# Performance work log

Measured on AMD Instinct MI355X. Metric: run time of the kernel, lower is better.

Reference implementation:

```python
import jax, jax.numpy as jnp
import numpy as np

B, S, D = 4, 4096, 1024
DD = 4 * D
N_EXPERTS = 8
CAPACITY = 1.0
LN_EPS = 1e-5


def setup_inputs() -> dict:
    key = jax.random.key(0)
    ks = jax.random.split(key, 8)
    s1 = 1.0 / np.sqrt(D)
    s2 = 1.0 / np.sqrt(DD)
    return {
        "x": jax.random.normal(ks[0], (B, S, D), jnp.float32),
        "gate_w": jax.random.normal(ks[1], (N_EXPERTS, D), jnp.float32) * 0.02,
        "ln_w": jnp.ones((D,), jnp.float32),
        "ln_b": jnp.zeros((D,), jnp.float32),
        "fc1s": jax.random.normal(ks[2], (N_EXPERTS, DD, D), jnp.float32) * s1,
        "b1s": jax.random.normal(ks[3], (N_EXPERTS, DD), jnp.float32) * s1,
        "fc2s": jax.random.normal(ks[4], (N_EXPERTS, D, DD), jnp.float32) * s2,
        "b2s": jax.random.normal(ks[5], (N_EXPERTS, D), jnp.float32) * s2,
    }


def reference(x, gate_w, ln_w, ln_b, fc1s, b1s, fc2s, b2s):
    og_shape = x.shape
    d = og_shape[-1]
    xf = x.reshape(-1, d)                       # (bs, d)
    bs = xf.shape[0]
    n = gate_w.shape[0]
    k = int(bs * CAPACITY) // n                 # static capacity per expert

    # softmax gating over experts
    scores = jax.nn.softmax(xf @ gate_w.T, axis=-1)   # (bs, n)

    # per-expert top-k tokens (column-wise descending sort, take first k)
    vals, idx = jax.lax.top_k(scores.T, k)      # (n, k)
    kept_w = vals.T                              # (k, n)
    kept_idx = idx.T                             # (k, n)
    flat_idx = kept_idx.reshape(-1)              # (k*n,) row-major: k outer, n inner

    # gather selected tokens, layernorm
    y = xf[flat_idx].reshape(k, n, d)            # (k, n, d)
    mu = y.mean(-1, keepdims=True)
    var = ((y - mu) ** 2).mean(-1, keepdims=True)
    y = (y - mu) * jax.lax.rsqrt(var + LN_EPS) * ln_w + ln_b

    # per-expert grouped GEMMs
    h = jnp.einsum('knd,nfd->knf', y, fc1s) + b1s          # (k, n, dd)
    h = jax.nn.gelu(h, approximate=True)                   # tanh gelu
    out = jnp.einsum('knf,ndf->knd', h, fc2s) + b2s        # (k, n, d)

    # weight by gate scores and scatter-add back onto the input tokens
    out = out * kept_w[..., None]
    xf = xf.at[flat_idx].add(out.reshape(k * n, d))
    return xf.reshape(og_shape)
```

## Files before the change

kernel.cpp:

```cpp
#include <hip/hip_runtime.h>

#define TOK  16384
#define NEXP 8
#define DIM  1024
#define DDIM 4096
#define KCAP 2048

typedef float  floatx4 __attribute__((ext_vector_type(4)));
typedef short  shortx8 __attribute__((ext_vector_type(8)));

static __device__ __forceinline__ unsigned short f2bf(float x) {
  unsigned u = __float_as_uint(x);
  return (unsigned short)((u + 0x7fffu + ((u >> 16) & 1u)) >> 16);
}

__global__ __launch_bounds__(256) void cvt_kernel(const float* __restrict__ src,
                                                  unsigned short* __restrict__ dst, int n4) {
  int i = blockIdx.x * 256 + threadIdx.x;
  if (i < n4) {
    float4 v = ((const float4*)src)[i];
    ushort4 o = make_ushort4(f2bf(v.x), f2bf(v.y), f2bf(v.z), f2bf(v.w));
    ((ushort4*)dst)[i] = o;
  }
}

__global__ __launch_bounds__(256) void gate_kernel(const float* __restrict__ x,
                                                   const float* __restrict__ gw,
                                                   float* __restrict__ scores) {
  __shared__ float gws[NEXP * DIM];
  int tid = threadIdx.x;
  for (int i = tid; i < NEXP * DIM / 4; i += 256)
    ((float4*)gws)[i] = ((const float4*)gw)[i];
  __syncthreads();
  int wave = tid >> 6, lane = tid & 63;
  int t = blockIdx.x * 4 + wave;
  const float4* xr = (const float4*)(x + (size_t)t * DIM);
  float4 xv[4];
#pragma unroll
  for (int j = 0; j < 4; ++j) xv[j] = xr[j * 64 + lane];
  float acc[NEXP];
#pragma unroll
  for (int e = 0; e < NEXP; ++e) acc[e] = 0.f;
#pragma unroll
  for (int e = 0; e < NEXP; ++e) {
    const float4* g4 = (const float4*)(gws + e * DIM);
#pragma unroll
    for (int j = 0; j < 4; ++j) {
      float4 g = g4[j * 64 + lane];
      acc[e] += xv[j].x * g.x + xv[j].y * g.y + xv[j].z * g.z + xv[j].w * g.w;
    }
  }
#pragma unroll
  for (int off = 32; off > 0; off >>= 1) {
#pragma unroll
    for (int e = 0; e < NEXP; ++e) acc[e] += __shfl_down(acc[e], off);
  }
  if (lane == 0) {
    float mx = acc[0];
#pragma unroll
    for (int e = 1; e < NEXP; ++e) mx = fmaxf(mx, acc[e]);
    float ex[NEXP], sum = 0.f;
#pragma unroll
    for (int e = 0; e < NEXP; ++e) { ex[e] = expf(acc[e] - mx); sum += ex[e]; }
    float inv = 1.f / sum;
#pragma unroll
    for (int e = 0; e < NEXP; ++e) scores[(size_t)e * TOK + t] = ex[e] * inv;
  }
}

#define TKT 1024
#define TKW (TKT / 64)
__global__ __launch_bounds__(TKT) void topk_kernel(const float* __restrict__ scores,
                                                   int* __restrict__ sel,
                                                   float* __restrict__ selw) {
  int e = blockIdx.x;
  const float* s = scores + (size_t)e * TOK;
  int tid = threadIdx.x, lane = tid & 63, wave = tid >> 6;
  __shared__ int cnt;
  __shared__ int wsum[TKW];

  unsigned prefix = 0;
  for (int bit = 30; bit >= 0; --bit) {
    unsigned cand = prefix | (1u << bit);
    if (tid == 0) cnt = 0;
    __syncthreads();
    int c = 0;
    for (int i = tid; i < TOK; i += TKT) c += (__float_as_uint(s[i]) >= cand) ? 1 : 0;
#pragma unroll
    for (int off = 32; off > 0; off >>= 1) c += __shfl_down(c, off);
    if (lane == 0) atomicAdd(&cnt, c);
    __syncthreads();
    if (cnt >= KCAP) prefix = cand;
    __syncthreads();
  }
  unsigned T = prefix;

  if (tid == 0) cnt = 0;
  __syncthreads();
  {
    int c = 0;
    for (int i = tid; i < TOK; i += TKT) c += (__float_as_uint(s[i]) > T) ? 1 : 0;
#pragma unroll
    for (int off = 32; off > 0; off >>= 1) c += __shfl_down(c, off);
    if (lane == 0) atomicAdd(&cnt, c);
  }
  __syncthreads();
  int n_gt = cnt;
  int need = KCAP - n_gt;

  __shared__ int pos;
  __shared__ int tiebase;
  if (tid == 0) { pos = 0; tiebase = 0; }
  __syncthreads();
  for (int chunk = 0; chunk < TOK; chunk += TKT) {
    int i = chunk + tid;
    unsigned v = __float_as_uint(s[i]);
    if (v > T) {
      int p = atomicAdd(&pos, 1);
      sel[e * KCAP + p]  = i;
      selw[e * KCAP + p] = __uint_as_float(v);
    }
    bool tie = (v == T);
    unsigned long long m = __ballot(tie);
    if (lane == 0) wsum[wave] = __popcll(m);
    __syncthreads();
    int base = tiebase;
    for (int w = 0; w < wave; ++w) base += wsum[w];
    int rank = base + __popcll(m & ((1ull << lane) - 1ull));
    if (tie && rank < need) {
      sel[e * KCAP + n_gt + rank]  = i;
      selw[e * KCAP + n_gt + rank] = __uint_as_float(T);
    }
    __syncthreads();
    if (tid == 0) {
      int tb = 0;
#pragma unroll
      for (int w = 0; w < TKW; ++w) tb += wsum[w];
      tiebase += tb;
    }
    __syncthreads();
  }
}

__global__ __launch_bounds__(256) void gather_ln_kernel(const float* __restrict__ x,
                                                        const int* __restrict__ sel,
                                                        const float* __restrict__ lnw,
                                                        const float* __restrict__ lnb,
                                                        unsigned short* __restrict__ Y) {
  int e = blockIdx.y, i = blockIdx.x;
  int tid = threadIdx.x, lane = tid & 63, wave = tid >> 6;
  int t = sel[e * KCAP + i];
  const float4* xr = (const float4*)(x + (size_t)t * DIM);
  float4 v = xr[tid];
  float s  = v.x + v.y + v.z + v.w;
  float sq = v.x * v.x + v.y * v.y + v.z * v.z + v.w * v.w;
#pragma unroll
  for (int off = 32; off > 0; off >>= 1) { s += __shfl_down(s, off); sq += __shfl_down(sq, off); }
  __shared__ float red[8];
  if (lane == 0) { red[wave] = s; red[4 + wave] = sq; }
  __syncthreads();
  s  = red[0] + red[1] + red[2] + red[3];
  sq = red[4] + red[5] + red[6] + red[7];
  float mu  = s * (1.f / DIM);
  float var = sq * (1.f / DIM) - mu * mu;
  float rs  = rsqrtf(var + 1e-5f);
  float4 w = ((const float4*)lnw)[tid];
  float4 b = ((const float4*)lnb)[tid];
  ushort4 o = make_ushort4(f2bf((v.x - mu) * rs * w.x + b.x),
                           f2bf((v.y - mu) * rs * w.y + b.y),
                           f2bf((v.z - mu) * rs * w.z + b.z),
                           f2bf((v.w - mu) * rs * w.w + b.w));
  ((ushort4*)(Y + ((size_t)e * KCAP + i) * DIM))[tid] = o;
}

#define BM  128
#define BN  128
#define BKT 64

template <int MODE>
__global__ __launch_bounds__(256) void gemm_kernel(
    const unsigned short* __restrict__ Aall,
    const unsigned short* __restrict__ Ball,
    const float* __restrict__ biasAll,
    int M, int N, int K,
    unsigned short* __restrict__ Hall,
    float* __restrict__ Out,
    const int* __restrict__ sel, const float* __restrict__ selw) {
  int e = blockIdx.z;
  const unsigned short* A = Aall + (size_t)e * M * K;
  const unsigned short* B = Ball + (size_t)e * N * K;
  const float* bias = biasAll + (size_t)e * N;

  __shared__ __align__(16) unsigned short As[BM * BKT];
  __shared__ __align__(16) unsigned short Bs[BN * BKT];
  __shared__ int   selS[BM];
  __shared__ float wS[BM];

  int tid = threadIdx.x, lane = tid & 63, wave = tid >> 6;
  int m0 = blockIdx.y * BM, n0 = blockIdx.x * BN;
  if (MODE == 2 && tid < BM) {
    selS[tid] = sel[e * KCAP + m0 + tid];
    wS[tid]   = selw[e * KCAP + m0 + tid];
  }
  int wm = (wave & 1) * 64, wn = (wave >> 1) * 64;
  int r8 = lane >> 3;
  int j8 = lane & 7;
  int scol = (j8 ^ r8) * 8;
  int row = lane & 15, quad = lane >> 4;
  int r7 = row & 7;

  floatx4 acc[4][4];
  floatx4 zero = {0.f, 0.f, 0.f, 0.f};
#pragma unroll
  for (int a = 0; a < 4; ++a)
#pragma unroll
    for (int b = 0; b < 4; ++b) acc[a][b] = zero;

  for (int k0 = 0; k0 < K; k0 += BKT) {
    __syncthreads();
#pragma unroll
    for (int j = 0; j < 4; ++j) {
      int q = wave * 4 + j;
      const unsigned short* ga = A + (size_t)(m0 + q * 8 + r8) * K + k0 + scol;
      __builtin_amdgcn_global_load_lds((const __attribute__((address_space(1))) void*)ga,
                                       (__attribute__((address_space(3))) void*)(As + q * 512),
                                       16, 0, 0);
      const unsigned short* gb = B + (size_t)(n0 + q * 8 + r8) * K + k0 + scol;
      __builtin_amdgcn_global_load_lds((const __attribute__((address_space(1))) void*)gb,
                                       (__attribute__((address_space(3))) void*)(Bs + q * 512),
                                       16, 0, 0);
    }
    __syncthreads();
#pragma unroll
    for (int kk = 0; kk < BKT; kk += 32) {
      int xg = ((quad + (kk >> 3)) ^ r7) << 3;
      shortx8 af[4], bf[4];
#pragma unroll
      for (int ti = 0; ti < 4; ++ti)
        af[ti] = *(const shortx8*)&As[(wm + ti * 16 + row) * BKT + xg];
#pragma unroll
      for (int tj = 0; tj < 4; ++tj)
        bf[tj] = *(const shortx8*)&Bs[(wn + tj * 16 + row) * BKT + xg];
#pragma unroll
      for (int ti = 0; ti < 4; ++ti)
#pragma unroll
        for (int tj = 0; tj < 4; ++tj)
          acc[ti][tj] = __builtin_amdgcn_mfma_f32_16x16x32_bf16(af[ti], bf[tj], acc[ti][tj], 0, 0, 0);
    }
  }

#pragma unroll
  for (int ti = 0; ti < 4; ++ti) {
#pragma unroll
    for (int tj = 0; tj < 4; ++tj) {
      int gn = n0 + wn + tj * 16 + row;
      float bb = bias[gn];
#pragma unroll
      for (int r = 0; r < 4; ++r) {
        int lrow = wm + ti * 16 + quad * 4 + r;
        float v = acc[ti][tj][r] + bb;
        if (MODE == 1) {
          float u = 0.7978845608028654f * (v + 0.044715f * v * v * v);
          u = fminf(u, 15.f);
          float e2 = __expf(2.f * u);
          float th = __fdividef(e2 - 1.f, e2 + 1.f);
          float g = 0.5f * v * (1.f + th);
          Hall[(size_t)e * M * N + (size_t)(m0 + lrow) * N + gn] = f2bf(g);
        } else {
          atomicAdd(&Out[(size_t)selS[lrow] * DIM + gn], wS[lrow] * v);
        }
      }
    }
  }
}

extern "C" void kernel_launch(void* const* d_in, const int* in_sizes, int n_in,
                              void* d_out, int out_size, void* d_ws, size_t ws_size,
                              hipStream_t stream) {
  const float* x   = (const float*)d_in[0];
  const float* gw  = (const float*)d_in[1];
  const float* lnw = (const float*)d_in[2];
  const float* lnb = (const float*)d_in[3];
  const float* fc1 = (const float*)d_in[4];
  const float* b1  = (const float*)d_in[5];
  const float* fc2 = (const float*)d_in[6];
  const float* b2  = (const float*)d_in[7];
  float* out = (float*)d_out;

  char* p = (char*)d_ws;
  float* scores = (float*)p;                 p += (size_t)NEXP * TOK * 4;
  int*   sel    = (int*)p;                   p += (size_t)NEXP * KCAP * 4;
  float* selw   = (float*)p;                 p += (size_t)NEXP * KCAP * 4;
  unsigned short* Wb = (unsigned short*)p;   p += (size_t)NEXP * DDIM * DIM * 2;
  unsigned short* Y  = (unsigned short*)p;   p += (size_t)NEXP * KCAP * DIM * 2;
  unsigned short* H  = (unsigned short*)p;   p += (size_t)NEXP * KCAP * DDIM * 2;

  hipMemcpyAsync(out, x, (size_t)TOK * DIM * sizeof(float), hipMemcpyDeviceToDevice, stream);

  gate_kernel<<<TOK / 4, 256, 0, stream>>>(x, gw, scores);
  topk_kernel<<<NEXP, TKT, 0, stream>>>(scores, sel, selw);
  gather_ln_kernel<<<dim3(KCAP, NEXP), 256, 0, stream>>>(x, sel, lnw, lnb, Y);

  const int n4w = NEXP * DDIM * DIM / 4;
  cvt_kernel<<<n4w / 256, 256, 0, stream>>>(fc1, Wb, n4w);
  gemm_kernel<1><<<dim3(DDIM / BN, KCAP / BM, NEXP), 256, 0, stream>>>(
      Y, Wb, b1, KCAP, DDIM, DIM, H, nullptr, nullptr, nullptr);

  cvt_kernel<<<n4w / 256, 256, 0, stream>>>(fc2, Wb, n4w);
  gemm_kernel<2><<<dim3(DIM / BN, KCAP / BM, NEXP), 256, 0, stream>>>(
      H, Wb, b2, KCAP, DIM, DDIM, nullptr, out, sel, selw);
}
```

Baseline: 926.9 us.

## Replace bitwise top-k search with radix histogram select, fuse output copy into gating

The gating kernel now also copies x into the output buffer and builds a per-expert 1024-bin histogram of score bit patterns with global atomics. The top-k threshold search runs as three radix passes (10 bits each) over that histogram, replacing the 31 sequential count passes. A separate device-to-device memcpy is removed. The tanh-GELU is rewritten as v*sigmoid(...) using exp2 and a fast reciprocal. Costs: histogram atomics contend because scores cluster in a few bins, and the fast GELU approximation changes precision slightly.

```diff
diff --git a/kernel.cpp b/kernel.cpp
--- a/kernel.cpp
+++ b/kernel.cpp
@@ -26,7 +26,9 @@
 
 __global__ __launch_bounds__(256) void gate_kernel(const float* __restrict__ x,
                                                    const float* __restrict__ gw,
-                                                   float* __restrict__ scores) {
+                                                   float* __restrict__ scores,
+                                                   unsigned* __restrict__ hist,
+                                                   float* __restrict__ out) {
   __shared__ float gws[NEXP * DIM];
   int tid = threadIdx.x;
   for (int i = tid; i < NEXP * DIM / 4; i += 256)
@@ -35,9 +37,12 @@
   int wave = tid >> 6, lane = tid & 63;
   int t = blockIdx.x * 4 + wave;
   const float4* xr = (const float4*)(x + (size_t)t * DIM);
+  float4* outw = (float4*)(out + (size_t)t * DIM);
   float4 xv[4];
 #pragma unroll
   for (int j = 0; j < 4; ++j) xv[j] = xr[j * 64 + lane];
+#pragma unroll
+  for (int j = 0; j < 4; ++j) outw[j * 64 + lane] = xv[j];
   float acc[NEXP];
 #pragma unroll
   for (int e = 0; e < NEXP; ++e) acc[e] = 0.f;
@@ -64,52 +69,84 @@
     for (int e = 0; e < NEXP; ++e) { ex[e] = expf(acc[e] - mx); sum += ex[e]; }
     float inv = 1.f / sum;
 #pragma unroll
-    for (int e = 0; e < NEXP; ++e) scores[(size_t)e * TOK + t] = ex[e] * inv;
+    for (int e = 0; e < NEXP; ++e) {
+      float sc = ex[e] * inv;
+      scores[(size_t)e * TOK + t] = sc;
+      atomicAdd(&hist[e * 1024 + (__float_as_uint(sc) >> 20)], 1u);
+    }
   }
 }
 
 #define TKT 1024
 #define TKW (TKT / 64)
-__global__ __launch_bounds__(TKT) void topk_kernel(const float* __restrict__ scores,
-                                                   int* __restrict__ sel,
-                                                   float* __restrict__ selw) {
+__global__ __launch_bounds__(TKT) void thresh_kernel(const float* __restrict__ scores,
+                                                     const unsigned* __restrict__ hist,
+                                                     int* __restrict__ sel,
+                                                     float* __restrict__ selw) {
   int e = blockIdx.x;
   const float* s = scores + (size_t)e * TOK;
   int tid = threadIdx.x, lane = tid & 63, wave = tid >> 6;
-  __shared__ int cnt;
+  __shared__ unsigned h[1024];
+  __shared__ int sh_b;
+
+  h[tid] = hist[e * 1024 + tid];
+  __syncthreads();
+  for (int d = 1; d < 1024; d <<= 1) {
+    unsigned tv = (tid + d < 1024) ? h[tid + d] : 0u;
+    __syncthreads();
+    h[tid] += tv;
+    __syncthreads();
+  }
+  if (h[tid] >= KCAP && (tid == 1023 || h[tid + 1] < (unsigned)KCAP)) sh_b = tid;
+  __syncthreads();
+  unsigned Tb = sh_b;
+  int n_gt = (Tb == 1023) ? 0 : (int)h[Tb + 1];
+  int need = KCAP - n_gt;
+  __syncthreads();
+
+  h[tid] = 0;
+  __syncthreads();
+  for (int i = tid; i < TOK; i += TKT) {
+    unsigned u = __float_as_uint(s[i]);
+    if ((u >> 20) == Tb) atomicAdd(&h[(u >> 10) & 1023], 1u);
+  }
+  __syncthreads();
+  for (int d = 1; d < 1024; d <<= 1) {
+    unsigned tv = (tid + d < 1024) ? h[tid + d] : 0u;
+    __syncthreads();
+    h[tid] += tv;
+    __syncthreads();
+  }
+  if (h[tid] >= (unsigned)need && (tid == 1023 || h[tid + 1] < (unsigned)need)) sh_b = tid;
+  __syncthreads();
+  unsigned Tb2 = sh_b;
+  n_gt += (Tb2 == 1023) ? 0 : (int)h[Tb2 + 1];
+  need = KCAP - n_gt;
+  __syncthreads();
+
+  unsigned midKey = (Tb << 10) | Tb2;
+  h[tid] = 0;
+  __syncthreads();
+  for (int i = tid; i < TOK; i += TKT) {
+    unsigned u = __float_as_uint(s[i]);
+    if ((u >> 10) == midKey) atomicAdd(&h[u & 1023], 1u);
+  }
+  __syncthreads();
+  for (int d = 1; d < 1024; d <<= 1) {
+    unsigned tv = (tid + d < 1024) ? h[tid + d] : 0u;
+    __syncthreads();
+    h[tid] += tv;
+    __syncthreads();
+  }
+  if (h[tid] >= (unsigned)need && (tid == 1023 || h[tid + 1] < (unsigned)need)) sh_b = tid;
+  __syncthreads();
+  unsigned Tb3 = sh_b;
+  n_gt += (Tb3 == 1023) ? 0 : (int)h[Tb3 + 1];
+  need = KCAP - n_gt;
+  unsigned T = (midKey << 10) | Tb3;
+
   __shared__ int wsum[TKW];
-
-  unsigned prefix = 0;
-  for (int bit = 30; bit >= 0; --bit) {
-    unsigned cand = prefix | (1u << bit);
-    if (tid == 0) cnt = 0;
-    __syncthreads();
-    int c = 0;
-    for (int i = tid; i < TOK; i += TKT) c += (__float_as_uint(s[i]) >= cand) ? 1 : 0;
-#pragma unroll
-    for (int off = 32; off > 0; off >>= 1) c += __shfl_down(c, off);
-    if (lane == 0) atomicAdd(&cnt, c);
-    __syncthreads();
-    if (cnt >= KCAP) prefix = cand;
-    __syncthreads();
-  }
-  unsigned T = prefix;
-
-  if (tid == 0) cnt = 0;
-  __syncthreads();
-  {
-    int c = 0;
-    for (int i = tid; i < TOK; i += TKT) c += (__float_as_uint(s[i]) > T) ? 1 : 0;
-#pragma unroll
-    for (int off = 32; off > 0; off >>= 1) c += __shfl_down(c, off);
-    if (lane == 0) atomicAdd(&cnt, c);
-  }
-  __syncthreads();
-  int n_gt = cnt;
-  int need = KCAP - n_gt;
-
-  __shared__ int pos;
-  __shared__ int tiebase;
+  __shared__ int pos, tiebase;
   if (tid == 0) { pos = 0; tiebase = 0; }
   __syncthreads();
   for (int chunk = 0; chunk < TOK; chunk += TKT) {
@@ -260,11 +297,10 @@
         int lrow = wm + ti * 16 + quad * 4 + r;
         float v = acc[ti][tj][r] + bb;
         if (MODE == 1) {
-          float u = 0.7978845608028654f * (v + 0.044715f * v * v * v);
-          u = fminf(u, 15.f);
-          float e2 = __expf(2.f * u);
-          float th = __fdividef(e2 - 1.f, e2 + 1.f);
-          float g = 0.5f * v * (1.f + th);
+          float p = v * v;
+          float z = v * fmaf(p, -0.10294422f, -2.30211836f);
+          float ex = __builtin_amdgcn_exp2f(z);
+          float g = v * __builtin_amdgcn_rcpf(1.f + ex);
           Hall[(size_t)e * M * N + (size_t)(m0 + lrow) * N + gn] = f2bf(g);
         } else {
           atomicAdd(&Out[(size_t)selS[lrow] * DIM + gn], wS[lrow] * v);
@@ -289,16 +325,17 @@
 
   char* p = (char*)d_ws;
   float* scores = (float*)p;                 p += (size_t)NEXP * TOK * 4;
+  unsigned* hist = (unsigned*)p;             p += (size_t)NEXP * 1024 * 4;
   int*   sel    = (int*)p;                   p += (size_t)NEXP * KCAP * 4;
   float* selw   = (float*)p;                 p += (size_t)NEXP * KCAP * 4;
   unsigned short* Wb = (unsigned short*)p;   p += (size_t)NEXP * DDIM * DIM * 2;
   unsigned short* Y  = (unsigned short*)p;   p += (size_t)NEXP * KCAP * DIM * 2;
   unsigned short* H  = (unsigned short*)p;   p += (size_t)NEXP * KCAP * DDIM * 2;
 
-  hipMemcpyAsync(out, x, (size_t)TOK * DIM * sizeof(float), hipMemcpyDeviceToDevice, stream);
-
-  gate_kernel<<<TOK / 4, 256, 0, stream>>>(x, gw, scores);
-  topk_kernel<<<NEXP, TKT, 0, stream>>>(scores, sel, selw);
+  hipMemsetAsync(hist, 0, (size_t)NEXP * 1024 * 4, stream);
+
+  gate_kernel<<<TOK / 4, 256, 0, stream>>>(x, gw, scores, hist, out);
+  thresh_kernel<<<NEXP, TKT, 0, stream>>>(scores, hist, sel, selw);
   gather_ln_kernel<<<dim3(KCAP, NEXP), 256, 0, stream>>>(x, sel, lnw, lnb, Y);
 
   const int n4w = NEXP * DDIM * DIM / 4;
```

Result: slower. 951.3 us (+2.6%).
